# Optimization experiments

Hardware: AMD Instinct MI355X
Metric: run time of the kernel (lower is better)

Reference implementation:

```python
import jax, jax.numpy as jnp
import numpy as np

NUM_LAYERS = 2
D = 128
H = 4
L = 16  # context window length
EPS = 1e-6


def _ln(x, g, b):
    mu = jnp.mean(x, -1, keepdims=True)
    v = jnp.mean((x - mu) ** 2, -1, keepdims=True)
    return (x - mu) / jnp.sqrt(v + EPS) * g + b


def _lin(x, W, b):
    # torch Linear / 1x1 Conv2d convention: W is [out, in]
    return jnp.einsum('...i,oi->...o', x, W) + b


def _context_attention(x, Lw):
    # x: [b, m, t, d]; front zero-pad time by Lw-1, sliding-window attention.
    # Note: padded zero keys get logit 0 and DO participate in the softmax
    # (faithful to the original, which does not mask the padding).
    b, m, t, d = x.shape
    xp = jnp.pad(x, ((0, 0), (0, 0), (Lw - 1, 0), (0, 0)))
    idx = jnp.arange(t)[:, None] + jnp.arange(Lw)[None, :]  # [t, Lw]
    win = xp[:, :, idx, :]                                   # [b,m,t,Lw,d]
    s = jnp.einsum('bmtd,bmtld->bmtl', x, win) / jnp.sqrt(jnp.asarray(d, x.dtype))
    w = jax.nn.softmax(s, -1)
    return jnp.einsum('bmtl,bmtld->bmtd', w, win)


def _mha(y, Wq, bq, Wk, bk, Wv, bv, Wfc, bfc):
    b, m, t, d = y.shape
    dk = d // H
    q = _lin(y, Wq, bq)   # 1x1 conv == pointwise linear
    k = _lin(y, Wk, bk)
    v = _lin(y, Wv, bv)
    cq = _context_attention(q, L).reshape(b, m, t, H, dk).transpose(0, 1, 3, 2, 4)
    ck = _context_attention(k, L).reshape(b, m, t, H, dk).transpose(0, 1, 3, 2, 4)
    vh = v.reshape(b, m, t, H, dk).transpose(0, 1, 3, 2, 4)  # [b,m,h,t,dk]
    scale = jnp.sqrt(jnp.asarray(dk, y.dtype))
    s = jnp.einsum('bmhqd,bmhkd->bmhqk', cq, ck) / scale
    a = jax.nn.softmax(s, -1)
    x = jnp.einsum('bmhqk,bmhkd->bmhqd', a, vh)   # [b,m,h,t,dk]
    x = x.transpose(0, 1, 3, 2, 4)                # [b,m,t,h,dk]
    # relation attention across assets m
    xr = x.transpose(0, 2, 3, 1, 4)               # [b,t,h,m,dk]
    sr = jnp.einsum('bthqd,bthkd->bthqk', xr, xr) / scale
    ar = jax.nn.softmax(sr, -1)
    xr = jnp.einsum('bthqk,bthkd->bthqd', ar, xr) # [b,t,h,m,dk]
    x = xr.transpose(0, 3, 1, 2, 4)               # [b,m,t,h,dk]
    return _lin(x.reshape(b, m, t, d), Wfc, bfc)


def setup_inputs() -> dict:
    key = jax.random.key(0)
    ks = jax.random.split(key, 16)
    sc = D ** -0.5
    NL = NUM_LAYERS
    inp = {
        'x':   jax.random.normal(ks[0], (2, 32, 512, D), jnp.float32),
        'Wq':  jax.random.normal(ks[1], (NL, D, D)) * sc,
        'bq':  jnp.zeros((NL, D)),
        'Wk':  jax.random.normal(ks[2], (NL, D, D)) * sc,
        'bk':  jnp.zeros((NL, D)),
        'Wv':  jax.random.normal(ks[3], (NL, D, D)) * sc,
        'bv':  jnp.zeros((NL, D)),
        'Wfc': jax.random.normal(ks[4], (NL, D, D)) * sc,
        'bfc': jnp.zeros((NL, D)),
        'W1':  jax.random.normal(ks[5], (NL, 4 * D, D)) * sc,
        'b1':  jnp.zeros((NL, 4 * D)),
        'W2':  jax.random.normal(ks[6], (NL, D, 4 * D)) * (4 * D) ** -0.5,
        'b2':  jnp.zeros((NL, D)),
        'g1':  jnp.ones((NL, D)),  'be1': jnp.zeros((NL, D)),
        'g2':  jnp.ones((NL, D)),  'be2': jnp.zeros((NL, D)),
        'gf':  jnp.ones((D,)),     'bef': jnp.zeros((D,)),
    }
    return inp


def reference(x, Wq, bq, Wk, bk, Wv, bv, Wfc, bfc, W1, b1, W2, b2,
              g1, be1, g2, be2, gf, bef):
    for i in range(NUM_LAYERS):
        # sublayer 0: pre-LN self-attention + residual (dropout=0)
        y = _mha(_ln(x, g1[i], be1[i]), Wq[i], bq[i], Wk[i], bk[i],
                 Wv[i], bv[i], Wfc[i], bfc[i])
        x = x + y
        # sublayer 1: pre-LN FFN + residual
        z = _ln(x, g2[i], be2[i])
        x = x + _lin(jax.nn.relu(_lin(z, W1[i], b1[i])), W2[i], b2[i])
    return _ln(x, gf, bef)
```

## Files before the change

kernel.cpp:

```cpp
#include <hip/hip_runtime.h>
#include <hip/hip_bf16.h>
#include <math.h>

#define B 2
#define M 32
#define T 512
#define D 128
#define H 4
#define DK 32
#define NTOK (B*M*T)

using s16x8 = __attribute__((ext_vector_type(8))) short;
using s16x4 = __attribute__((ext_vector_type(4))) short;
using f32x4 = __attribute__((ext_vector_type(4))) float;

__device__ __forceinline__ short f2bf(float x) {
    union { float f; unsigned u; } a; a.f = x;
    unsigned r = a.u + 0x7fffu + ((a.u >> 16) & 1u);
    return (short)(r >> 16);
}
__device__ __forceinline__ unsigned pkbf(float lo, float hi) {
    union { __hip_bfloat162 h; unsigned u; } c;
    c.h = __float22bfloat162_rn(float2{lo, hi});
    return c.u;
}

__global__ __launch_bounds__(256) void cvt_all_kernel(const float* __restrict__ Wq, const float* __restrict__ Wk,
                                                      const float* __restrict__ Wv, const float* __restrict__ Wfc,
                                                      const float* __restrict__ W1, const float* __restrict__ W2,
                                                      short* __restrict__ dst)
{
    int i = (blockIdx.x * 256 + threadIdx.x) * 4;
    if (i >= 393216) return;
    const float* src; int off;
    if (i < 131072) {
        int wsel = i >> 15; off = i & 32767;
        src = (wsel == 0) ? Wq : (wsel == 1) ? Wk : (wsel == 2) ? Wv : Wfc;
    } else if (i < 262144) { src = W1; off = i - 131072; }
    else                   { src = W2; off = i - 262144; }
    float4 v = *(const float4*)(src + off);
    ushort4 u;
    u.x = (unsigned short)f2bf(v.x); u.y = (unsigned short)f2bf(v.y);
    u.z = (unsigned short)f2bf(v.z); u.w = (unsigned short)f2bf(v.w);
    *(ushort4*)(dst + i) = u;
}

__global__ __launch_bounds__(256) void ln_kernel(const float* __restrict__ in, float* __restrict__ outf,
                                                 const float* __restrict__ g, const float* __restrict__ b)
{
    int wave = threadIdx.x >> 6;
    int lane = threadIdx.x & 63;
    int row  = blockIdx.x * 4 + wave;
    const float* rp = in + (size_t)row * D;
    float v0 = rp[lane], v1 = rp[lane + 64];
    float s = v0 + v1, ss = v0 * v0 + v1 * v1;
    #pragma unroll
    for (int off = 32; off; off >>= 1) { s += __shfl_xor(s, off); ss += __shfl_xor(ss, off); }
    float mu  = s * (1.0f / 128.0f);
    float var = ss * (1.0f / 128.0f) - mu * mu;
    float rs  = rsqrtf(var + 1e-6f);
    float* op = outf + (size_t)row * D;
    op[lane]      = (v0 - mu) * rs * g[lane]      + b[lane];
    op[lane + 64] = (v1 - mu) * rs * g[lane + 64] + b[lane + 64];
}

#define KP 136

#define LN_STAGE(XPTR, GPTR, BEPTR)                                              \
    {                                                                            \
        const float* xp = (XPTR) + (size_t)(rowBase + sr) * D + sq * 32;         \
        float4 xv[8];                                                            \
        _Pragma("unroll")                                                        \
        for (int j = 0; j < 8; j++) xv[j] = *(const float4*)(xp + j * 4);        \
        float s = 0.0f, ss = 0.0f;                                               \
        _Pragma("unroll")                                                        \
        for (int j = 0; j < 8; j++) {                                            \
            s  += xv[j].x + xv[j].y + xv[j].z + xv[j].w;                         \
            ss += xv[j].x*xv[j].x + xv[j].y*xv[j].y + xv[j].z*xv[j].z + xv[j].w*xv[j].w; \
        }                                                                        \
        s  += __shfl_xor(s, 1);  s  += __shfl_xor(s, 2);                         \
        ss += __shfl_xor(ss, 1); ss += __shfl_xor(ss, 2);                        \
        float mu  = s * (1.0f / 128.0f);                                         \
        float var = ss * (1.0f / 128.0f) - mu * mu;                              \
        float rs  = rsqrtf(var + 1e-6f);                                         \
        const float* gp  = (GPTR) + sq * 32;                                     \
        const float* bep = (BEPTR) + sq * 32;                                    \
        short* asd = &As[sr * KP + sq * 32];                                     \
        _Pragma("unroll")                                                        \
        for (int c = 0; c < 4; c++) {                                            \
            float4 a0 = xv[2*c], a1 = xv[2*c+1];                                 \
            float4 g0 = *(const float4*)(gp + c * 8);                            \
            float4 g1 = *(const float4*)(gp + c * 8 + 4);                        \
            float4 b0 = *(const float4*)(bep + c * 8);                           \
            float4 b1 = *(const float4*)(bep + c * 8 + 4);                       \
            union { unsigned u[4]; s16x8 v8; } pu;                               \
            pu.u[0] = pkbf((a0.x-mu)*rs*g0.x+b0.x, (a0.y-mu)*rs*g0.y+b0.y);      \
            pu.u[1] = pkbf((a0.z-mu)*rs*g0.z+b0.z, (a0.w-mu)*rs*g0.w+b0.w);      \
            pu.u[2] = pkbf((a1.x-mu)*rs*g1.x+b1.x, (a1.y-mu)*rs*g1.y+b1.y);      \
            pu.u[3] = pkbf((a1.z-mu)*rs*g1.z+b1.z, (a1.w-mu)*rs*g1.w+b1.w);      \
            *(s16x8*)(asd + c * 8) = pu.v8;                                      \
        }                                                                        \
    }

__global__ __launch_bounds__(512) void qkv_ln_kernel(const float* __restrict__ X,
                                                     const float* __restrict__ g, const float* __restrict__ be,
                                                     const short* __restrict__ Wq, const short* __restrict__ Wk,
                                                     const short* __restrict__ Wv,
                                                     const float* __restrict__ bq, const float* __restrict__ bk,
                                                     const float* __restrict__ bv,
                                                     short* __restrict__ Qo, short* __restrict__ Ko,
                                                     short* __restrict__ Vo)
{
    __shared__ short As[128 * KP];
    __shared__ short Ws[128 * KP];
    const int tid = threadIdx.x;
    const int rowBase = blockIdx.x * 128;
    const int sr = tid >> 2, sq = tid & 3;
    const int w = tid >> 6, l = tid & 63;
    const int lg = l >> 4, lr = l & 15;
    const int wr = w >> 2, wc = w & 3;

    LN_STAGE(X, g, be)

    const short* wsrc[3] = { Wq, Wk, Wv };
    const float* bsrc[3] = { bq, bk, bv };
    short*       osrc[3] = { Qo, Ko, Vo };

    for (int gsel = 0; gsel < 3; gsel++) {
        s16x8 wv4[4];
        const short* wp = wsrc[gsel] + (size_t)sr * D + sq * 32;
        #pragma unroll
        for (int i = 0; i < 4; i++) wv4[i] = *(const s16x8*)(wp + i * 8);
        __syncthreads();
        short* wsd = &Ws[sr * KP + sq * 32];
        #pragma unroll
        for (int i = 0; i < 4; i++) *(s16x8*)(wsd + i * 8) = wv4[i];
        __syncthreads();

        f32x4 acc[4][2];
        #pragma unroll
        for (int qi = 0; qi < 4; qi++)
            #pragma unroll
            for (int nj = 0; nj < 2; nj++)
                acc[qi][nj] = (f32x4){0.0f, 0.0f, 0.0f, 0.0f};
        #pragma unroll
        for (int kk = 0; kk < 4; kk++) {
            s16x8 af[4], bfr[2];
            #pragma unroll
            for (int qi = 0; qi < 4; qi++)
                af[qi] = *(const s16x8*)&As[(wr * 64 + qi * 16 + lr) * KP + kk * 32 + lg * 8];
            #pragma unroll
            for (int nj = 0; nj < 2; nj++)
                bfr[nj] = *(const s16x8*)&Ws[(wc * 32 + nj * 16 + lr) * KP + kk * 32 + lg * 8];
            #pragma unroll
            for (int qi = 0; qi < 4; qi++)
                #pragma unroll
                for (int nj = 0; nj < 2; nj++)
                    acc[qi][nj] = __builtin_amdgcn_mfma_f32_16x16x32_bf16(af[qi], bfr[nj], acc[qi][nj], 0, 0, 0);
        }
        #pragma unroll
        for (int nj = 0; nj < 2; nj++) {
            int col = wc * 32 + nj * 16 + lr;
            float bb = bsrc[gsel][col];
            #pragma unroll
            for (int qi = 0; qi < 4; qi++) {
                #pragma unroll
                for (int rr = 0; rr < 4; rr++) {
                    int row = rowBase + wr * 64 + qi * 16 + lg * 4 + rr;
                    osrc[gsel][(size_t)row * D + col] = f2bf(acc[qi][nj][rr] + bb);
                }
            }
        }
    }
}

__global__ __launch_bounds__(512) void mlp1_ln_kernel(const float* __restrict__ X,
                                                      const float* __restrict__ g, const float* __restrict__ be,
                                                      const short* __restrict__ W1, const float* __restrict__ b1,
                                                      short* __restrict__ Hb)
{
    __shared__ short As[128 * KP];
    __shared__ short Ws[128 * KP];
    const int tid = threadIdx.x;
    const int rowBase = blockIdx.x * 128;
    const int sr = tid >> 2, sq = tid & 3;
    const int w = tid >> 6, l = tid & 63;
    const int lg = l >> 4, lr = l & 15;
    const int wr = w >> 2, wc = w & 3;

    LN_STAGE(X, g, be)

    for (int ct = 0; ct < 4; ct++) {
        s16x8 wv4[4];
        const short* wp = W1 + (size_t)(ct * 128 + sr) * D + sq * 32;
        #pragma unroll
        for (int i = 0; i < 4; i++) wv4[i] = *(const s16x8*)(wp + i * 8);
        __syncthreads();
        short* wsd = &Ws[sr * KP + sq * 32];
        #pragma unroll
        for (int i = 0; i < 4; i++) *(s16x8*)(wsd + i * 8) = wv4[i];
        __syncthreads();

        f32x4 acc[4][2];
        #pragma unroll
        for (int qi = 0; qi < 4; qi++)
            #pragma unroll
            for (int nj = 0; nj < 2; nj++)
                acc[qi][nj] = (f32x4){0.0f, 0.0f, 0.0f, 0.0f};
        #pragma unroll
        for (int kk = 0; kk < 4; kk++) {
            s16x8 af[4], bfr[2];
            #pragma unroll
            for (int qi = 0; qi < 4; qi++)
                af[qi] = *(const s16x8*)&As[(wr * 64 + qi * 16 + lr) * KP + kk * 32 + lg * 8];
            #pragma unroll
            for (int nj = 0; nj < 2; nj++)
                bfr[nj] = *(const s16x8*)&Ws[(wc * 32 + nj * 16 + lr) * KP + kk * 32 + lg * 8];
            #pragma unroll
            for (int qi = 0; qi < 4; qi++)
                #pragma unroll
                for (int nj = 0; nj < 2; nj++)
                    acc[qi][nj] = __builtin_amdgcn_mfma_f32_16x16x32_bf16(af[qi], bfr[nj], acc[qi][nj], 0, 0, 0);
        }
        #pragma unroll
        for (int nj = 0; nj < 2; nj++) {
            int col = ct * 128 + wc * 32 + nj * 16 + lr;
            float bb = b1[col];
            #pragma unroll
            for (int qi = 0; qi < 4; qi++) {
                #pragma unroll
                for (int rr = 0; rr < 4; rr++) {
                    int row = rowBase + wr * 64 + qi * 16 + lg * 4 + rr;
                    Hb[(size_t)row * 512 + col] = f2bf(fmaxf(acc[qi][nj][rr] + bb, 0.0f));
                }
            }
        }
    }
}

template<int DIN>
__global__ __launch_bounds__(512) void gemm_bf16_kernel(const short* __restrict__ A, const short* __restrict__ W,
                                                        const float* __restrict__ bias, const float* __restrict__ res,
                                                        float* __restrict__ outf, int Dout)
{
    __shared__ short As[128 * KP];
    __shared__ short Ws[128 * KP];
    const int tid = threadIdx.x;
    const int rowBase = blockIdx.y * 128;
    const int colBase = blockIdx.x * 128;
    const int sr = tid >> 2, sq = tid & 3;
    const int w = tid >> 6, l = tid & 63;
    const int lg = l >> 4, lr = l & 15;
    const int wr = w >> 2, wc = w & 3;

    f32x4 acc[4][2];
    #pragma unroll
    for (int qi = 0; qi < 4; qi++)
        #pragma unroll
        for (int nj = 0; nj < 2; nj++)
            acc[qi][nj] = (f32x4){0.0f, 0.0f, 0.0f, 0.0f};

    const short* ap = A + (size_t)(rowBase + sr) * DIN + sq * 32;
    const short* wp = W + (size_t)(colBase + sr) * DIN + sq * 32;
    short* asd = &As[sr * KP + sq * 32];
    short* wsd = &Ws[sr * KP + sq * 32];

    #pragma unroll
    for (int kt = 0; kt < DIN / 128; kt++) {
        s16x8 av[4], wv[4];
        #pragma unroll
        for (int i = 0; i < 4; i++) {
            av[i] = *(const s16x8*)(ap + kt * 128 + i * 8);
            wv[i] = *(const s16x8*)(wp + kt * 128 + i * 8);
        }
        if (kt) __syncthreads();
        #pragma unroll
        for (int i = 0; i < 4; i++) {
            *(s16x8*)(asd + i * 8) = av[i];
            *(s16x8*)(wsd + i * 8) = wv[i];
        }
        __syncthreads();
        #pragma unroll
        for (int kk = 0; kk < 4; kk++) {
            s16x8 af[4], bfr[2];
            #pragma unroll
            for (int qi = 0; qi < 4; qi++)
                af[qi] = *(const s16x8*)&As[(wr * 64 + qi * 16 + lr) * KP + kk * 32 + lg * 8];
            #pragma unroll
            for (int nj = 0; nj < 2; nj++)
                bfr[nj] = *(const s16x8*)&Ws[(wc * 32 + nj * 16 + lr) * KP + kk * 32 + lg * 8];
            #pragma unroll
            for (int qi = 0; qi < 4; qi++)
                #pragma unroll
                for (int nj = 0; nj < 2; nj++)
                    acc[qi][nj] = __builtin_amdgcn_mfma_f32_16x16x32_bf16(af[qi], bfr[nj], acc[qi][nj], 0, 0, 0);
        }
    }

    #pragma unroll
    for (int nj = 0; nj < 2; nj++) {
        int col = colBase + wc * 32 + nj * 16 + lr;
        float bb = bias[col];
        #pragma unroll
        for (int qi = 0; qi < 4; qi++) {
            #pragma unroll
            for (int rr = 0; rr < 4; rr++) {
                int row = rowBase + wr * 64 + qi * 16 + lg * 4 + rr;
                size_t o = (size_t)row * Dout + col;
                outf[o] = acc[qi][nj][rr] + bb + res[o];
            }
        }
    }
}

#define XSP 136
#define XTP 84
__global__ __launch_bounds__(256) void ctx_mfma_kernel(const short* __restrict__ in0, short* __restrict__ out0,
                                                       const short* __restrict__ in1, short* __restrict__ out1)
{
    __shared__ short Xs[80 * XSP];
    __shared__ short Xt[128 * XTP];

    const short* in  = blockIdx.y ? in1 : in0;
    short*       out = blockIdx.y ? out1 : out0;
    int bm = blockIdx.x >> 3;
    int t0 = (blockIdx.x & 7) * 64;
    int tid = threadIdx.x;
    const short* base = in + (size_t)bm * T * D;

    #pragma unroll
    for (int it = 0; it < 5; it++) {
        int idx = it * 256 + tid;
        int row = idx >> 4, c16 = idx & 15;
        int t = t0 - 16 + row;
        s16x8 v = {0, 0, 0, 0, 0, 0, 0, 0};
        if (t >= 0) v = *(const s16x8*)(base + (size_t)t * D + c16 * 8);
        *(s16x8*)&Xs[row * XSP + c16 * 8] = v;
    }
    __syncthreads();
    #pragma unroll
    for (int it = 0; it < 5; it++) {
        int task = it * 256 + tid;
        int g = task / 80, row = task % 80;
        s16x8 v = *(const s16x8*)&Xs[row * XSP + g * 8];
        #pragma unroll
        for (int j = 0; j < 8; j++) Xt[(g * 8 + j) * XTP + row] = v[j];
    }
    __syncthreads();

    int w = tid >> 6, l = tid & 63;
    int lg = l >> 4, lr = l & 15;
    f32x4 zacc = {0.0f, 0.0f, 0.0f, 0.0f};
    const float C1 = 0.0883883476483184f * 1.4426950408889634f;

    s16x8 qf[4];
    #pragma unroll
    for (int kd = 0; kd < 4; kd++)
        qf[kd] = *(const s16x8*)&Xs[(16 + w * 16 + lr) * XSP + kd * 32 + lg * 8];

    f32x4 sacc[2];
    #pragma unroll
    for (int s = 0; s < 2; s++) {
        f32x4 a = zacc;
        #pragma unroll
        for (int kd = 0; kd < 4; kd++) {
            s16x8 kf = *(const s16x8*)&Xs[(w * 16 + s * 16 + lr) * XSP + kd * 32 + lg * 8];
            a = __builtin_amdgcn_mfma_f32_16x16x32_bf16(kf, qf[kd], a, 0, 0, 0);
        }
        sacc[s] = a;
    }

    float p[2][4];
    float mx = -1e30f;
    #pragma unroll
    for (int s = 0; s < 2; s++)
        #pragma unroll
        for (int r = 0; r < 4; r++) {
            int dlt = s * 16 + lg * 4 + r - 16 - lr;
            float val = (dlt >= -15 && dlt <= 0) ? sacc[s][r] : -1e30f;
            p[s][r] = val;
            mx = fmaxf(mx, val);
        }
    mx = fmaxf(mx, __shfl_xor(mx, 16));
    mx = fmaxf(mx, __shfl_xor(mx, 32));
    float mc = mx * C1;
    float ps = 0.0f;
    #pragma unroll
    for (int s = 0; s < 2; s++)
        #pragma unroll
        for (int r = 0; r < 4; r++) {
            float e = exp2f(fmaf(p[s][r], C1, -mc));
            p[s][r] = e;
            ps += e;
        }
    ps += __shfl_xor(ps, 16);
    ps += __shfl_xor(ps, 32);

    union { unsigned u[4]; s16x8 v8; } pu;
    pu.u[0] = pkbf(p[0][0], p[0][1]);
    pu.u[1] = pkbf(p[0][2], p[0][3]);
    pu.u[2] = pkbf(p[1][0], p[1][1]);
    pu.u[3] = pkbf(p[1][2], p[1][3]);
    s16x8 pf = pu.v8;

    float rl = 1.0f / ps;
    short* op = out + (size_t)(bm * T + t0 + w * 16 + lr) * D;
    #pragma unroll
    for (int dt = 0; dt < 8; dt++) {
        const short* vb = &Xt[(dt * 16 + lr) * XTP + w * 16 + lg * 4];
        s16x4 a = *(const s16x4*)(vb);
        s16x4 b = *(const s16x4*)(vb + 16);
        s16x8 vf = __builtin_shufflevector(a, b, 0, 1, 2, 3, 4, 5, 6, 7);
        f32x4 Oa = __builtin_amdgcn_mfma_f32_16x16x32_bf16(vf, pf, zacc, 0, 0, 0);
        union { unsigned u[2]; ushort4 s4; } ou;
        ou.u[0] = pkbf(Oa[0] * rl, Oa[1] * rl);
        ou.u[1] = pkbf(Oa[2] * rl, Oa[3] * rl);
        *(ushort4*)(op + dt * 16 + lg * 4) = ou.s4;
    }
}

#define KPAD 40
#define VTP  520
__global__ __launch_bounds__(1024) void attn_mfma_kernel(const short* __restrict__ q, const short* __restrict__ k,
                                                         const short* __restrict__ v, short* __restrict__ out)
{
    __shared__ short Ks[512 * KPAD];
    __shared__ short Vt[32 * VTP];

    int h  = blockIdx.x & 3;
    int bm = blockIdx.x >> 2;
    int tid = threadIdx.x;
    size_t headoff = (size_t)(bm * T) * D + h * DK;

    {
        int row = tid >> 1, half = tid & 1;
        const s16x8* kp8 = (const s16x8*)(k + headoff + (size_t)row * D + half * 16);
        s16x8 k0 = kp8[0], k1 = kp8[1];
        short* kd = &Ks[row * KPAD + half * 16];
        *(s16x8*)(kd)     = k0;
        *(s16x8*)(kd + 8) = k1;
        const s16x8* vp8 = (const s16x8*)(v + headoff + (size_t)row * D + half * 16);
        s16x8 v0 = vp8[0], v1 = vp8[1];
        #pragma unroll
        for (int d = 0; d < 8; d++) {
            Vt[(half * 16 + d) * VTP + row]     = v0[d];
            Vt[(half * 16 + 8 + d) * VTP + row] = v1[d];
        }
    }
    __syncthreads();

    int w = tid >> 6, l = tid & 63;
    int lg = l >> 4, lr = l & 15;
    int qw = w * 32;

    s16x8 qf[2];
    #pragma unroll
    for (int qi = 0; qi < 2; qi++)
        qf[qi] = *(const s16x8*)(q + headoff + (size_t)(qw + qi * 16 + lr) * D + lg * 8);

    f32x4 Oa[2][2];
    float lrow[2];
    #pragma unroll
    for (int qi = 0; qi < 2; qi++) {
        lrow[qi] = 0.0f;
        #pragma unroll
        for (int r = 0; r < 4; r++) { Oa[qi][0][r] = 0.0f; Oa[qi][1][r] = 0.0f; }
    }
    const float C1 = 0.17677669529663689f * 1.4426950408889634f;
    f32x4 zacc = {0.0f, 0.0f, 0.0f, 0.0f};

    for (int kt = 0; kt < 8; kt++) {
        int kb = kt * 64;
        s16x8 kf[2][2];
        #pragma unroll
        for (int s = 0; s < 2; s++)
            #pragma unroll
            for (int hh = 0; hh < 2; hh++)
                kf[s][hh] = *(const s16x8*)&Ks[(kb + s * 32 + hh * 16 + lr) * KPAD + lg * 8];
        s16x8 vf[2][2];
        #pragma unroll
        for (int dh = 0; dh < 2; dh++)
            #pragma unroll
            for (int s = 0; s < 2; s++) {
                const short* vb = &Vt[(dh * 16 + lr) * VTP + kb + s * 32 + lg * 4];
                s16x4 a = *(const s16x4*)(vb);
                s16x4 b = *(const s16x4*)(vb + 16);
                vf[dh][s] = __builtin_shufflevector(a, b, 0, 1, 2, 3, 4, 5, 6, 7);
            }
        #pragma unroll
        for (int qi = 0; qi < 2; qi++) {
            f32x4 sa[2][2];
            #pragma unroll
            for (int s = 0; s < 2; s++)
                #pragma unroll
                for (int hh = 0; hh < 2; hh++)
                    sa[s][hh] = __builtin_amdgcn_mfma_f32_16x16x32_bf16(kf[s][hh], qf[qi], zacc, 0, 0, 0);
            float p[2][8];
            float ps = 0.0f;
            #pragma unroll
            for (int s = 0; s < 2; s++)
                #pragma unroll
                for (int hh = 0; hh < 2; hh++)
                    #pragma unroll
                    for (int r = 0; r < 4; r++) {
                        float e = exp2f(sa[s][hh][r] * C1);
                        p[s][hh * 4 + r] = e;
                        ps += e;
                    }
            lrow[qi] += ps;
            s16x8 pf[2];
            #pragma unroll
            for (int s = 0; s < 2; s++) {
                union { unsigned u[4]; s16x8 v8; } pu;
                pu.u[0] = pkbf(p[s][0], p[s][1]);
                pu.u[1] = pkbf(p[s][2], p[s][3]);
                pu.u[2] = pkbf(p[s][4], p[s][5]);
                pu.u[3] = pkbf(p[s][6], p[s][7]);
                pf[s] = pu.v8;
            }
            #pragma unroll
            for (int dh = 0; dh < 2; dh++)
                #pragma unroll
                for (int s = 0; s < 2; s++)
                    Oa[qi][dh] = __builtin_amdgcn_mfma_f32_16x16x32_bf16(vf[dh][s], pf[s], Oa[qi][dh], 0, 0, 0);
        }
    }

    #pragma unroll
    for (int qi = 0; qi < 2; qi++) {
        float lv = lrow[qi];
        lv += __shfl_xor(lv, 16);
        lv += __shfl_xor(lv, 32);
        float rl = 1.0f / lv;
        int qrow = qw + qi * 16 + lr;
        short* op = out + headoff + (size_t)qrow * D;
        #pragma unroll
        for (int dh = 0; dh < 2; dh++) {
            union { unsigned u[2]; ushort4 s4; } ou;
            ou.u[0] = pkbf(Oa[qi][dh][0] * rl, Oa[qi][dh][1] * rl);
            ou.u[1] = pkbf(Oa[qi][dh][2] * rl, Oa[qi][dh][3] * rl);
            *(ushort4*)(op + dh * 16 + lg * 4) = ou.s4;
        }
    }
}

#define CXP 136
#define CTP 36
__global__ __launch_bounds__(256) void crossm_mfma_kernel(const short* __restrict__ in, short* __restrict__ out)
{
    __shared__ short Xs[32 * CXP];
    __shared__ short Xt[128 * CTP];
    int b = blockIdx.x >> 9;
    int t = blockIdx.x & 511;
    int tid = threadIdx.x;

    #pragma unroll
    for (int it = 0; it < 2; it++) {
        int idx = it * 256 + tid;
        int m = idx >> 4, c16 = idx & 15;
        s16x8 v = *(const s16x8*)(in + (size_t)((b * M + m) * T + t) * D + c16 * 8);
        *(s16x8*)&Xs[m * CXP + c16 * 8] = v;
    }
    __syncthreads();
    #pragma unroll
    for (int it = 0; it < 2; it++) {
        int task = it * 256 + tid;
        int g = task >> 5, m = task & 31;
        s16x8 v = *(const s16x8*)&Xs[m * CXP + g * 8];
        #pragma unroll
        for (int j = 0; j < 8; j++) Xt[(g * 8 + j) * CTP + m] = v[j];
    }
    __syncthreads();

    int h = tid >> 6, l = tid & 63;
    int lg = l >> 4, lr = l & 15;
    f32x4 zacc = {0.0f, 0.0f, 0.0f, 0.0f};
    const float C1 = 0.17677669529663689f * 1.4426950408889634f;

    s16x8 xf[2];
    #pragma unroll
    for (int i = 0; i < 2; i++)
        xf[i] = *(const s16x8*)&Xs[(i * 16 + lr) * CXP + h * 32 + lg * 8];

    f32x4 sacc[2][2];
    #pragma unroll
    for (int kt = 0; kt < 2; kt++)
        #pragma unroll
        for (int qt = 0; qt < 2; qt++)
            sacc[kt][qt] = __builtin_amdgcn_mfma_f32_16x16x32_bf16(xf[kt], xf[qt], zacc, 0, 0, 0);

    s16x8 pf[2];
    float rl[2];
    #pragma unroll
    for (int qt = 0; qt < 2; qt++) {
        float p[2][4];
        float ps = 0.0f;
        #pragma unroll
        for (int kt = 0; kt < 2; kt++)
            #pragma unroll
            for (int r = 0; r < 4; r++) {
                float e = exp2f(sacc[kt][qt][r] * C1);
                p[kt][r] = e;
                ps += e;
            }
        ps += __shfl_xor(ps, 16);
        ps += __shfl_xor(ps, 32);
        rl[qt] = 1.0f / ps;
        union { unsigned u[4]; s16x8 v8; } pu;
        pu.u[0] = pkbf(p[0][0], p[0][1]);
        pu.u[1] = pkbf(p[0][2], p[0][3]);
        pu.u[2] = pkbf(p[1][0], p[1][1]);
        pu.u[3] = pkbf(p[1][2], p[1][3]);
        pf[qt] = pu.v8;
    }

    #pragma unroll
    for (int qt = 0; qt < 2; qt++) {
        int qm = qt * 16 + lr;
        short* op = out + (size_t)((b * M + qm) * T + t) * D + h * 32;
        #pragma unroll
        for (int dt = 0; dt < 2; dt++) {
            const short* vb = &Xt[(h * 32 + dt * 16 + lr) * CTP + lg * 4];
            s16x4 a = *(const s16x4*)(vb);
            s16x4 bb = *(const s16x4*)(vb + 16);
            s16x8 vf = __builtin_shufflevector(a, bb, 0, 1, 2, 3, 4, 5, 6, 7);
            f32x4 Oa = __builtin_amdgcn_mfma_f32_16x16x32_bf16(vf, pf[qt], zacc, 0, 0, 0);
            union { unsigned u[2]; ushort4 s4; } ou;
            ou.u[0] = pkbf(Oa[0] * rl[qt], Oa[1] * rl[qt]);
            ou.u[1] = pkbf(Oa[2] * rl[qt], Oa[3] * rl[qt]);
            *(ushort4*)(op + dt * 16 + lg * 4) = ou.s4;
        }
    }
}

extern "C" void kernel_launch(void* const* d_in, const int* in_sizes, int n_in,
                              void* d_out, int out_size, void* d_ws, size_t ws_size,
                              hipStream_t stream)
{
    (void)in_sizes; (void)n_in; (void)out_size; (void)ws_size;
    const float* xin = (const float*)d_in[0];
    const float* Wq  = (const float*)d_in[1];
    const float* bq  = (const float*)d_in[2];
    const float* Wk  = (const float*)d_in[3];
    const float* bk  = (const float*)d_in[4];
    const float* Wv  = (const float*)d_in[5];
    const float* bv  = (const float*)d_in[6];
    const float* Wfc = (const float*)d_in[7];
    const float* bfc = (const float*)d_in[8];
    const float* W1  = (const float*)d_in[9];
    const float* b1  = (const float*)d_in[10];
    const float* W2  = (const float*)d_in[11];
    const float* b2  = (const float*)d_in[12];
    const float* g1  = (const float*)d_in[13];
    const float* be1 = (const float*)d_in[14];
    const float* g2  = (const float*)d_in[15];
    const float* be2 = (const float*)d_in[16];
    const float* gf  = (const float*)d_in[17];
    const float* bef = (const float*)d_in[18];

    float* X = (float*)d_out;
    char* wsb = (char*)d_ws;
    const size_t SEGB = (size_t)NTOK * D * sizeof(float);
    const size_t SEGH = SEGB / 2;
    short* Qpb = (short*)(wsb + SEGH);
    short* Kpb = (short*)(wsb + 2 * SEGH);
    short* Vbf = (short*)(wsb + 3 * SEGH);
    short* CQb = (short*)(wsb + 4 * SEGH);
    short* CKb = (short*)(wsb + 5 * SEGH);
    short* Hbf = (short*)(wsb);

    short* Wall = (short*)(wsb + 6 * SEGH);
    short* Wqb  = Wall;
    short* Wkb  = Wall + 32768;
    short* Wvb  = Wall + 65536;
    short* Wfcb = Wall + 98304;
    short* W1b  = Wall + 131072;
    short* W2b  = Wall + 262144;

    cvt_all_kernel<<<384, 256, 0, stream>>>(Wq, Wk, Wv, Wfc, W1, W2, Wall);

    for (int i = 0; i < 2; i++) {
        const float* xi  = i ? X : xin;
        qkv_ln_kernel<<<NTOK / 128, 512, 0, stream>>>(xi, g1 + i * D, be1 + i * D,
                                                      Wqb + i * D * D, Wkb + i * D * D, Wvb + i * D * D,
                                                      bq + i * D, bk + i * D, bv + i * D,
                                                      Qpb, Kpb, Vbf);
        ctx_mfma_kernel<<<dim3(B * M * (T / 64), 2), 256, 0, stream>>>(Qpb, CQb, Kpb, CKb);
        attn_mfma_kernel<<<B * M * H, 1024, 0, stream>>>(CQb, CKb, Vbf, Qpb);
        crossm_mfma_kernel<<<B * T, 256, 0, stream>>>(Qpb, Kpb);
        gemm_bf16_kernel<128><<<dim3(1, NTOK / 128), 512, 0, stream>>>(Kpb, Wfcb + i * D * D, bfc + i * D, xi, X, D);
        mlp1_ln_kernel<<<NTOK / 128, 512, 0, stream>>>(X, g2 + i * D, be2 + i * D,
                                                       W1b + i * 4 * D * D, b1 + i * 4 * D, Hbf);
        gemm_bf16_kernel<512><<<dim3(1, NTOK / 128), 512, 0, stream>>>(Hbf, W2b + i * 4 * D * D, b2 + i * D, X, X, D);
    }
    ln_kernel<<<NTOK / 4, 256, 0, stream>>>(X, X, gf, bef);
}
```

Baseline: 231.1 us.

## Shrink GEMM row tiles to 64 and read weight fragments directly from global

The four projection GEMM kernels (QKV+LN, FFN1+LN, FC, W2) are rewritten around a shared macro. Each uses 64-row tiles and 256 threads, and each wave loads its weight fragments straight from global memory into registers instead of staging them through shared memory. This removes the per-tile weight LDS copy and its barriers, and doubles the block count so more compute units get work. The W2 kernel now stages the full 512-wide activation row block in a larger LDS buffer. The cost is that every block rereads the weights from L2, and the larger LDS footprint in W2 may lower occupancy.

```diff
diff --git a/kernel.cpp b/kernel.cpp
--- a/kernel.cpp
+++ b/kernel.cpp
@@ -102,7 +102,28 @@
         }                                                                        \
     }
 
-__global__ __launch_bounds__(512) void qkv_ln_kernel(const float* __restrict__ X,
+#define GEMM64_CORE(WPTR, WLD, KTOFF)                                            \
+    {                                                                            \
+        _Pragma("unroll")                                                        \
+        for (int nj = 0; nj < 2; nj++)                                           \
+            _Pragma("unroll")                                                    \
+            for (int kk = 0; kk < 4; kk++)                                       \
+                bfr[nj][kk] = *(const s16x8*)((WPTR) + (size_t)(w * 32 + nj * 16 + lr) * (WLD) + (KTOFF) + kk * 32 + lg * 8); \
+        _Pragma("unroll")                                                        \
+        for (int kk = 0; kk < 4; kk++) {                                         \
+            s16x8 af[4];                                                         \
+            _Pragma("unroll")                                                    \
+            for (int qi = 0; qi < 4; qi++)                                       \
+                af[qi] = *(const s16x8*)&As[(qi * 16 + lr) * ASLD + (KTOFF) + kk * 32 + lg * 8]; \
+            _Pragma("unroll")                                                    \
+            for (int qi = 0; qi < 4; qi++)                                       \
+                _Pragma("unroll")                                                \
+                for (int nj = 0; nj < 2; nj++)                                   \
+                    acc[qi][nj] = __builtin_amdgcn_mfma_f32_16x16x32_bf16(af[qi], bfr[nj][kk], acc[qi][nj], 0, 0, 0); \
+        }                                                                        \
+    }
+
+__global__ __launch_bounds__(256) void qkv_ln_kernel(const float* __restrict__ X,
                                                      const float* __restrict__ g, const float* __restrict__ be,
                                                      const short* __restrict__ Wq, const short* __restrict__ Wk,
                                                      const short* __restrict__ Wv,
@@ -111,147 +132,111 @@
                                                      short* __restrict__ Qo, short* __restrict__ Ko,
                                                      short* __restrict__ Vo)
 {
-    __shared__ short As[128 * KP];
-    __shared__ short Ws[128 * KP];
+    #define ASLD KP
+    __shared__ short As[64 * KP];
     const int tid = threadIdx.x;
-    const int rowBase = blockIdx.x * 128;
+    const int rowBase = blockIdx.x * 64;
     const int sr = tid >> 2, sq = tid & 3;
     const int w = tid >> 6, l = tid & 63;
     const int lg = l >> 4, lr = l & 15;
-    const int wr = w >> 2, wc = w & 3;
 
     LN_STAGE(X, g, be)
+    __syncthreads();
 
     const short* wsrc[3] = { Wq, Wk, Wv };
     const float* bsrc[3] = { bq, bk, bv };
     short*       osrc[3] = { Qo, Ko, Vo };
 
     for (int gsel = 0; gsel < 3; gsel++) {
-        s16x8 wv4[4];
-        const short* wp = wsrc[gsel] + (size_t)sr * D + sq * 32;
-        #pragma unroll
-        for (int i = 0; i < 4; i++) wv4[i] = *(const s16x8*)(wp + i * 8);
-        __syncthreads();
-        short* wsd = &Ws[sr * KP + sq * 32];
-        #pragma unroll
-        for (int i = 0; i < 4; i++) *(s16x8*)(wsd + i * 8) = wv4[i];
-        __syncthreads();
-
         f32x4 acc[4][2];
         #pragma unroll
         for (int qi = 0; qi < 4; qi++)
             #pragma unroll
             for (int nj = 0; nj < 2; nj++)
                 acc[qi][nj] = (f32x4){0.0f, 0.0f, 0.0f, 0.0f};
-        #pragma unroll
-        for (int kk = 0; kk < 4; kk++) {
-            s16x8 af[4], bfr[2];
-            #pragma unroll
-            for (int qi = 0; qi < 4; qi++)
-                af[qi] = *(const s16x8*)&As[(wr * 64 + qi * 16 + lr) * KP + kk * 32 + lg * 8];
-            #pragma unroll
-            for (int nj = 0; nj < 2; nj++)
-                bfr[nj] = *(const s16x8*)&Ws[(wc * 32 + nj * 16 + lr) * KP + kk * 32 + lg * 8];
-            #pragma unroll
-            for (int qi = 0; qi < 4; qi++)
-                #pragma unroll
-                for (int nj = 0; nj < 2; nj++)
-                    acc[qi][nj] = __builtin_amdgcn_mfma_f32_16x16x32_bf16(af[qi], bfr[nj], acc[qi][nj], 0, 0, 0);
-        }
+        s16x8 bfr[2][4];
+        GEMM64_CORE(wsrc[gsel], D, 0)
+
         #pragma unroll
         for (int nj = 0; nj < 2; nj++) {
-            int col = wc * 32 + nj * 16 + lr;
+            int col = w * 32 + nj * 16 + lr;
             float bb = bsrc[gsel][col];
             #pragma unroll
             for (int qi = 0; qi < 4; qi++) {
                 #pragma unroll
                 for (int rr = 0; rr < 4; rr++) {
-                    int row = rowBase + wr * 64 + qi * 16 + lg * 4 + rr;
+                    int row = rowBase + qi * 16 + lg * 4 + rr;
                     osrc[gsel][(size_t)row * D + col] = f2bf(acc[qi][nj][rr] + bb);
                 }
             }
         }
     }
-}
-
-__global__ __launch_bounds__(512) void mlp1_ln_kernel(const float* __restrict__ X,
+    #undef ASLD
+}
+
+__global__ __launch_bounds__(256) void mlp1_ln_kernel(const float* __restrict__ X,
                                                       const float* __restrict__ g, const float* __restrict__ be,
                                                       const short* __restrict__ W1, const float* __restrict__ b1,
                                                       short* __restrict__ Hb)
 {
-    __shared__ short As[128 * KP];
-    __shared__ short Ws[128 * KP];
+    #define ASLD KP
+    __shared__ short As[64 * KP];
     const int tid = threadIdx.x;
-    const int rowBase = blockIdx.x * 128;
+    const int rowBase = blockIdx.x * 64;
     const int sr = tid >> 2, sq = tid & 3;
     const int w = tid >> 6, l = tid & 63;
     const int lg = l >> 4, lr = l & 15;
-    const int wr = w >> 2, wc = w & 3;
 
     LN_STAGE(X, g, be)
+    __syncthreads();
 
     for (int ct = 0; ct < 4; ct++) {
-        s16x8 wv4[4];
-        const short* wp = W1 + (size_t)(ct * 128 + sr) * D + sq * 32;
-        #pragma unroll
-        for (int i = 0; i < 4; i++) wv4[i] = *(const s16x8*)(wp + i * 8);
-        __syncthreads();
-        short* wsd = &Ws[sr * KP + sq * 32];
-        #pragma unroll
-        for (int i = 0; i < 4; i++) *(s16x8*)(wsd + i * 8) = wv4[i];
-        __syncthreads();
-
         f32x4 acc[4][2];
         #pragma unroll
         for (int qi = 0; qi < 4; qi++)
             #pragma unroll
             for (int nj = 0; nj < 2; nj++)
                 acc[qi][nj] = (f32x4){0.0f, 0.0f, 0.0f, 0.0f};
-        #pragma unroll
-        for (int kk = 0; kk < 4; kk++) {
-            s16x8 af[4], bfr[2];
-            #pragma unroll
-            for (int qi = 0; qi < 4; qi++)
-                af[qi] = *(const s16x8*)&As[(wr * 64 + qi * 16 + lr) * KP + kk * 32 + lg * 8];
-            #pragma unroll
-            for (int nj = 0; nj < 2; nj++)
-                bfr[nj] = *(const s16x8*)&Ws[(wc * 32 + nj * 16 + lr) * KP + kk * 32 + lg * 8];
-            #pragma unroll
-            for (int qi = 0; qi < 4; qi++)
-                #pragma unroll
-                for (int nj = 0; nj < 2; nj++)
-                    acc[qi][nj] = __builtin_amdgcn_mfma_f32_16x16x32_bf16(af[qi], bfr[nj], acc[qi][nj], 0, 0, 0);
-        }
+        s16x8 bfr[2][4];
+        const short* wp = W1 + (size_t)(ct * 128) * D;
+        GEMM64_CORE(wp, D, 0)
+
         #pragma unroll
         for (int nj = 0; nj < 2; nj++) {
-            int col = ct * 128 + wc * 32 + nj * 16 + lr;
+            int col = ct * 128 + w * 32 + nj * 16 + lr;
             float bb = b1[col];
             #pragma unroll
             for (int qi = 0; qi < 4; qi++) {
                 #pragma unroll
                 for (int rr = 0; rr < 4; rr++) {
-                    int row = rowBase + wr * 64 + qi * 16 + lg * 4 + rr;
+                    int row = rowBase + qi * 16 + lg * 4 + rr;
                     Hb[(size_t)row * 512 + col] = f2bf(fmaxf(acc[qi][nj][rr] + bb, 0.0f));
                 }
             }
         }
     }
-}
-
-template<int DIN>
-__global__ __launch_bounds__(512) void gemm_bf16_kernel(const short* __restrict__ A, const short* __restrict__ W,
-                                                        const float* __restrict__ bias, const float* __restrict__ res,
-                                                        float* __restrict__ outf, int Dout)
-{
-    __shared__ short As[128 * KP];
-    __shared__ short Ws[128 * KP];
+    #undef ASLD
+}
+
+__global__ __launch_bounds__(256) void fc_gemm_kernel(const short* __restrict__ A, const short* __restrict__ W,
+                                                      const float* __restrict__ bias, const float* __restrict__ res,
+                                                      float* __restrict__ outf)
+{
+    #define ASLD KP
+    __shared__ short As[64 * KP];
     const int tid = threadIdx.x;
-    const int rowBase = blockIdx.y * 128;
-    const int colBase = blockIdx.x * 128;
+    const int rowBase = blockIdx.x * 64;
     const int sr = tid >> 2, sq = tid & 3;
     const int w = tid >> 6, l = tid & 63;
     const int lg = l >> 4, lr = l & 15;
-    const int wr = w >> 2, wc = w & 3;
+
+    {
+        const short* ap = A + (size_t)(rowBase + sr) * D + sq * 32;
+        short* asd = &As[sr * KP + sq * 32];
+        #pragma unroll
+        for (int i = 0; i < 4; i++) *(s16x8*)(asd + i * 8) = *(const s16x8*)(ap + i * 8);
+    }
+    __syncthreads();
 
     f32x4 acc[4][2];
     #pragma unroll
@@ -259,58 +244,74 @@
         #pragma unroll
         for (int nj = 0; nj < 2; nj++)
             acc[qi][nj] = (f32x4){0.0f, 0.0f, 0.0f, 0.0f};
-
-    const short* ap = A + (size_t)(rowBase + sr) * DIN + sq * 32;
-    const short* wp = W + (size_t)(colBase + sr) * DIN + sq * 32;
-    short* asd = &As[sr * KP + sq * 32];
-    short* wsd = &Ws[sr * KP + sq * 32];
-
-    #pragma unroll
-    for (int kt = 0; kt < DIN / 128; kt++) {
-        s16x8 av[4], wv[4];
-        #pragma unroll
-        for (int i = 0; i < 4; i++) {
-            av[i] = *(const s16x8*)(ap + kt * 128 + i * 8);
-            wv[i] = *(const s16x8*)(wp + kt * 128 + i * 8);
-        }
-        if (kt) __syncthreads();
-        #pragma unroll
-        for (int i = 0; i < 4; i++) {
-            *(s16x8*)(asd + i * 8) = av[i];
-            *(s16x8*)(wsd + i * 8) = wv[i];
-        }
-        __syncthreads();
-        #pragma unroll
-        for (int kk = 0; kk < 4; kk++) {
-            s16x8 af[4], bfr[2];
-            #pragma unroll
-            for (int qi = 0; qi < 4; qi++)
-                af[qi] = *(const s16x8*)&As[(wr * 64 + qi * 16 + lr) * KP + kk * 32 + lg * 8];
-            #pragma unroll
-            for (int nj = 0; nj < 2; nj++)
-                bfr[nj] = *(const s16x8*)&Ws[(wc * 32 + nj * 16 + lr) * KP + kk * 32 + lg * 8];
-            #pragma unroll
-            for (int qi = 0; qi < 4; qi++)
-                #pragma unroll
-                for (int nj = 0; nj < 2; nj++)
-                    acc[qi][nj] = __builtin_amdgcn_mfma_f32_16x16x32_bf16(af[qi], bfr[nj], acc[qi][nj], 0, 0, 0);
-        }
-    }
+    s16x8 bfr[2][4];
+    GEMM64_CORE(W, D, 0)
 
     #pragma unroll
     for (int nj = 0; nj < 2; nj++) {
-        int col = colBase + wc * 32 + nj * 16 + lr;
+        int col = w * 32 + nj * 16 + lr;
         float bb = bias[col];
         #pragma unroll
         for (int qi = 0; qi < 4; qi++) {
             #pragma unroll
             for (int rr = 0; rr < 4; rr++) {
-                int row = rowBase + wr * 64 + qi * 16 + lg * 4 + rr;
-                size_t o = (size_t)row * Dout + col;
+                int row = rowBase + qi * 16 + lg * 4 + rr;
+                size_t o = (size_t)row * D + col;
                 outf[o] = acc[qi][nj][rr] + bb + res[o];
             }
         }
     }
+    #undef ASLD
+}
+
+#define KP5 520
+__global__ __launch_bounds__(256) void w2_gemm_kernel(const short* __restrict__ A, const short* __restrict__ W,
+                                                      const float* __restrict__ bias, const float* __restrict__ res,
+                                                      float* __restrict__ outf)
+{
+    #define ASLD KP5
+    __shared__ short As[64 * KP5];
+    const int tid = threadIdx.x;
+    const int rowBase = blockIdx.x * 64;
+    const int sr = tid >> 2, sq = tid & 3;
+    const int w = tid >> 6, l = tid & 63;
+    const int lg = l >> 4, lr = l & 15;
+
+    {
+        const short* ap = A + (size_t)(rowBase + sr) * 512 + sq * 128;
+        short* asd = &As[sr * KP5 + sq * 128];
+        #pragma unroll
+        for (int i = 0; i < 16; i++) *(s16x8*)(asd + i * 8) = *(const s16x8*)(ap + i * 8);
+    }
+    __syncthreads();
+
+    f32x4 acc[4][2];
+    #pragma unroll
+    for (int qi = 0; qi < 4; qi++)
+        #pragma unroll
+        for (int nj = 0; nj < 2; nj++)
+            acc[qi][nj] = (f32x4){0.0f, 0.0f, 0.0f, 0.0f};
+    #pragma unroll
+    for (int kt = 0; kt < 4; kt++) {
+        s16x8 bfr[2][4];
+        GEMM64_CORE(W, 512, kt * 128)
+    }
+
+    #pragma unroll
+    for (int nj = 0; nj < 2; nj++) {
+        int col = w * 32 + nj * 16 + lr;
+        float bb = bias[col];
+        #pragma unroll
+        for (int qi = 0; qi < 4; qi++) {
+            #pragma unroll
+            for (int rr = 0; rr < 4; rr++) {
+                int row = rowBase + qi * 16 + lg * 4 + rr;
+                size_t o = (size_t)row * D + col;
+                outf[o] = acc[qi][nj][rr] + bb + res[o];
+            }
+        }
+    }
+    #undef ASLD
 }
 
 #define XSP 136
@@ -681,17 +682,17 @@
 
     for (int i = 0; i < 2; i++) {
         const float* xi  = i ? X : xin;
-        qkv_ln_kernel<<<NTOK / 128, 512, 0, stream>>>(xi, g1 + i * D, be1 + i * D,
-                                                      Wqb + i * D * D, Wkb + i * D * D, Wvb + i * D * D,
-                                                      bq + i * D, bk + i * D, bv + i * D,
-                                                      Qpb, Kpb, Vbf);
+        qkv_ln_kernel<<<NTOK / 64, 256, 0, stream>>>(xi, g1 + i * D, be1 + i * D,
+                                                     Wqb + i * D * D, Wkb + i * D * D, Wvb + i * D * D,
+                                                     bq + i * D, bk + i * D, bv + i * D,
+                                                     Qpb, Kpb, Vbf);
         ctx_mfma_kernel<<<dim3(B * M * (T / 64), 2), 256, 0, stream>>>(Qpb, CQb, Kpb, CKb);
         attn_mfma_kernel<<<B * M * H, 1024, 0, stream>>>(CQb, CKb, Vbf, Qpb);
         crossm_mfma_kernel<<<B * T, 256, 0, stream>>>(Qpb, Kpb);
-        gemm_bf16_kernel<128><<<dim3(1, NTOK / 128), 512, 0, stream>>>(Kpb, Wfcb + i * D * D, bfc + i * D, xi, X, D);
-        mlp1_ln_kernel<<<NTOK / 128, 512, 0, stream>>>(X, g2 + i * D, be2 + i * D,
-                                                       W1b + i * 4 * D * D, b1 + i * 4 * D, Hbf);
-        gemm_bf16_kernel<512><<<dim3(1, NTOK / 128), 512, 0, stream>>>(Hbf, W2b + i * 4 * D * D, b2 + i * D, X, X, D);
+        fc_gemm_kernel<<<NTOK / 64, 256, 0, stream>>>(Kpb, Wfcb + i * D * D, bfc + i * D, xi, X);
+        mlp1_ln_kernel<<<NTOK / 64, 256, 0, stream>>>(X, g2 + i * D, be2 + i * D,
+                                                      W1b + i * 4 * D * D, b1 + i * 4 * D, Hbf);
+        w2_gemm_kernel<<<NTOK / 64, 256, 0, stream>>>(Hbf, W2b + i * 4 * D * D, b2 + i * D, X, X);
     }
     ln_kernel<<<NTOK / 4, 256, 0, stream>>>(X, X, gf, bef);
 }
```

Result: slower. 260.4 us (+12.7%).
